# Performance work log

Measured on AMD Instinct MI355X. Metric: run time of the kernel, lower is better.

## Reference

```python
import jax, jax.numpy as jnp
import numpy as np

B, C, IMG, P = 32, 3, 224, 16
D, H, L, F, NCLS = 768, 12, 12, 3072, 1000
NP = (IMG // P) ** 2  # 196
DH = D // H  # 64
EPS = 1e-5


def _ln(x, g, b):
    m = jnp.mean(x, axis=-1, keepdims=True)
    v = jnp.mean(jnp.square(x - m), axis=-1, keepdims=True)
    return (x - m) * jax.lax.rsqrt(v + EPS) * g + b


def setup_inputs() -> dict:
    key = jax.random.key(0)
    ks = iter(jax.random.split(key, 32))
    s = 0.02
    rn = lambda shape: jax.random.normal(next(ks), shape, dtype=jnp.float32) * s
    inp = {
        "x": jax.random.normal(next(ks), (B, C, IMG, IMG), dtype=jnp.float32),
        "Wp": rn((P * P * C, D)), "bp": jnp.zeros((D,), jnp.float32),
        "cls": rn((1, 1, D)), "pos": rn((1, NP + 1, D)),
        # per-layer stacked params (leading dim L)
        "ln1_g": jnp.ones((L, D), jnp.float32), "ln1_b": jnp.zeros((L, D), jnp.float32),
        "Wq": rn((L, H, D, DH)), "bq": jnp.zeros((L, H, DH), jnp.float32),
        "Wk": rn((L, H, D, DH)), "bk": jnp.zeros((L, H, DH), jnp.float32),
        "Wv": rn((L, H, D, DH)), "bv": jnp.zeros((L, H, DH), jnp.float32),
        "Wo": rn((L, D, D)), "bo": jnp.zeros((L, D), jnp.float32),
        "ln2_g": jnp.ones((L, D), jnp.float32), "ln2_b": jnp.zeros((L, D), jnp.float32),
        "W1": rn((L, D, F)), "b1": jnp.zeros((L, F), jnp.float32),
        "W2": rn((L, F, D)), "b2": jnp.zeros((L, D), jnp.float32),
        # classification head
        "hln_g": jnp.ones((D,), jnp.float32), "hln_b": jnp.zeros((D,), jnp.float32),
        "hW1": rn((D, D)), "hb1": jnp.zeros((D,), jnp.float32),
        "hW2": rn((D, NCLS)), "hb2": jnp.zeros((NCLS,), jnp.float32),
    }
    return inp


def _vit(x, Wp, bp, cls, pos, ln1_g, ln1_b, Wq, bq, Wk, bk, Wv, bv, Wo, bo,
         ln2_g, ln2_b, W1, b1, W2, b2, hln_g, hln_b, hW1, hb1, hW2, hb2):
    b = x.shape[0]
    g = IMG // P
    # nn.Unfold(k=16, s=16): channel order (c, kh, kw), patch order (ph, pw)
    patches = x.reshape(b, C, g, P, g, P).transpose(0, 2, 4, 1, 3, 5).reshape(b, NP, C * P * P)
    h = patches @ Wp + bp  # [b, NP, D]
    h = jnp.concatenate([jnp.broadcast_to(cls, (b, 1, D)), h], axis=1) + pos  # [b, S, D]

    scale = 1.0 / jnp.sqrt(jnp.asarray(DH, h.dtype))

    def step(h, p):
        g1, b1_, wq, bq_, wk, bk_, wv, bv_, wo, bo_, g2, b2_, w1, bb1, w2, bb2 = p
        xn = _ln(h, g1, b1_)
        q = jnp.einsum('bsd,hde->bhse', xn, wq) + bq_[:, None, :]
        k = jnp.einsum('bsd,hde->bhse', xn, wk) + bk_[:, None, :]
        v = jnp.einsum('bsd,hde->bhse', xn, wv) + bv_[:, None, :]
        scores = jnp.einsum('bhse,bhte->bhst', q, k) * scale
        attn = jax.nn.softmax(scores, axis=-1)
        o = jnp.einsum('bhst,bhte->bhse', attn, v)  # [b,H,S,DH]
        o = o.transpose(0, 2, 1, 3).reshape(b, -1, D)  # concat heads
        h = o @ wo + bo_ + h
        xn = _ln(h, g2, b2_)
        h = jax.nn.gelu(xn @ w1 + bb1, approximate=False) @ w2 + bb2 + h
        return h, None

    params = (ln1_g, ln1_b, Wq, bq, Wk, bk, Wv, bv, Wo, bo, ln2_g, ln2_b, W1, b1, W2, b2)
    h, _ = jax.lax.scan(step, h, params)

    c = h[:, 0, :]
    c = _ln(c, hln_g, hln_b)
    return jax.nn.gelu(c @ hW1 + hb1, approximate=False) @ hW2 + hb2


def reference(x, Wp, bp, cls, pos, ln1_g, ln1_b, Wq, bq, Wk, bk, Wv, bv, Wo, bo,
              ln2_g, ln2_b, W1, b1, W2, b2, hln_g, hln_b, hW1, hb1, hW2, hb2):
    return _vit(x, Wp, bp, cls, pos, ln1_g, ln1_b, Wq, bq, Wk, bk, Wv, bv, Wo, bo,
                ln2_g, ln2_b, W1, b1, W2, b2, hln_g, hln_b, hW1, hb1, hW2, hb2)
```

## Files before the change

### kernel.cpp

```cpp
#include <hip/hip_runtime.h>

typedef unsigned short u16;
typedef __attribute__((ext_vector_type(8))) short short8;
typedef __attribute__((ext_vector_type(4))) float f32x4;

#define NTOK 6304
#define SP 197

#define OFF_WQKVT 0L
#define OFF_WOT   42467328L
#define OFF_W1T   56623104L
#define OFF_W2T   113246208L
#define OFF_WPT   169869312L
#define OFF_BQKV  171048960L
#define OFF_H     171159552L
#define OFF_XN    190525440L
#define OFF_QKV   200208384L
#define OFF_SC    229257216L
#define OFF_PM1   288867840L
#define OFF_VT    327599616L
#define OFF_CN    340182528L
#define OFF_T1    340280832L
#define WS_NEEDED 340379136L

__device__ __forceinline__ u16 f2bf(float x) {
  unsigned int u = __float_as_uint(x);
  u += 0x7fffu + ((u >> 16) & 1u);
  return (u16)(u >> 16);
}

__device__ __forceinline__ float gelu_f(float x) {
  return 0.5f * x * (1.0f + erff(x * 0.70710678118654752f));
}

__device__ __forceinline__ void gload_lds16(const void* g, void* l) {
  __builtin_amdgcn_global_load_lds(
      (const __attribute__((address_space(1))) unsigned int*)g,
      (__attribute__((address_space(3))) unsigned int*)l, 16, 0, 0);
}

template <int BM, int BN, int WM, int WN, bool BIAS, bool GELU, bool RES,
          bool OBF16, bool REMAP>
__global__ __launch_bounds__(WM * WN * 64, 2) void gemm2(
    const u16* __restrict__ A, int lda,
    const u16* __restrict__ Bm, int ldb,
    void* Cv, int ldc,
    const float* __restrict__ bias, const float* res, int ldres,
    int M, int N, int K, int tilesN) {
  constexpr int THREADS = WM * WN * 64;
  constexpr int TM = BM / WM, TN = BN / WN;
  constexpr int FM = TM / 16, FN = TN / 16;
  constexpr int APT = (BM * 8) / THREADS;
  constexpr int BPT = (BN * 8) / THREADS;
  constexpr int ABYTES = BM * 128;
  constexpr int BUF = ABYTES + BN * 128;
  __shared__ __align__(16) char smem[2 * BUF];

  const int t = threadIdx.x;
  const int l = t & 63;
  const int lr = l & 15, kb = (l >> 4) & 3;
  const int wid = t >> 6;
  const int wr = wid / WN, wc = wid % WN;

  const int nwg = gridDim.x;
  const int orig = blockIdx.x;
  const int q8 = nwg >> 3, r8 = nwg & 7;
  const int xcd = orig & 7, loc = orig >> 3;
  const int wg =
      (xcd < r8 ? xcd * (q8 + 1) : r8 * (q8 + 1) + (xcd - r8) * q8) + loc;
  const int tn = wg % tilesN, tm = wg / tilesN;
  const int m0 = tm * BM, n0 = tn * BN;
  const int Mm1 = M - 1, Nm1 = N - 1;

  const f32x4 zf = {0.f, 0.f, 0.f, 0.f};
  f32x4 acc[FM][FN];
#pragma unroll
  for (int fm = 0; fm < FM; ++fm)
#pragma unroll
    for (int fn = 0; fn < FN; ++fn) acc[fm][fn] = zf;

  auto stage = [&](int kt, int d) {
    const int k0 = kt << 6;
    char* base = smem + d * BUF;
#pragma unroll
    for (int p = 0; p < APT; ++p) {
      int idx = p * THREADS + t;
      int r = idx >> 3, cl = idx & 7;
      int rr = m0 + r;
      rr = rr > Mm1 ? Mm1 : rr;
      gload_lds16(A + (long)rr * lda + k0 + ((cl ^ (r & 7)) << 3),
                  base + ((p * THREADS + (t & ~63)) << 4));
    }
    char* bbase = base + ABYTES;
#pragma unroll
    for (int p = 0; p < BPT; ++p) {
      int idx = p * THREADS + t;
      int r = idx >> 3, cl = idx & 7;
      int rr = n0 + r;
      rr = rr > Nm1 ? Nm1 : rr;
      gload_lds16(Bm + (long)rr * ldb + k0 + ((cl ^ (r & 7)) << 3),
                  bbase + ((p * THREADS + (t & ~63)) << 4));
    }
  };

  const int nt = K >> 6;
  stage(0, 0);
  __syncthreads();

  for (int kt = 0; kt < nt; ++kt) {
    if (kt + 1 < nt) stage(kt + 1, (kt + 1) & 1);
    const char* Ab = smem + (kt & 1) * BUF;
    const char* Bb = Ab + ABYTES;
#pragma unroll
    for (int kk = 0; kk < 2; ++kk) {
      const int ch = ((((kk << 2) | kb) ^ (lr & 7)) << 4);
      short8 af[FM], bf[FN];
#pragma unroll
      for (int fm = 0; fm < FM; ++fm)
        af[fm] = *(const short8*)(Ab + (wr * TM + fm * 16 + lr) * 128 + ch);
#pragma unroll
      for (int fn = 0; fn < FN; ++fn)
        bf[fn] = *(const short8*)(Bb + (wc * TN + fn * 16 + lr) * 128 + ch);
#pragma unroll
      for (int fm = 0; fm < FM; ++fm)
#pragma unroll
        for (int fn = 0; fn < FN; ++fn)
          acc[fm][fn] = __builtin_amdgcn_mfma_f32_16x16x32_bf16(af[fm], bf[fn],
                                                                acc[fm][fn], 0, 0, 0);
    }
    __syncthreads();
  }

#pragma unroll
  for (int fn = 0; fn < FN; ++fn) {
    const int gc = n0 + wc * TN + fn * 16 + lr;
    if (gc >= N) continue;
    const float bv = BIAS ? bias[gc] : 0.0f;
#pragma unroll
    for (int fm = 0; fm < FM; ++fm) {
#pragma unroll
      for (int j = 0; j < 4; ++j) {
        const int gr = m0 + wr * TM + fm * 16 + kb * 4 + j;
        if (gr >= M) continue;
        float v = acc[fm][fn][j] + bv;
        if (RES) v += res[(long)gr * ldres + gc];
        if (GELU) v = gelu_f(v);
        long orow = gr;
        if (REMAP) orow = (long)(gr / 196) * 197 + (gr % 196) + 1;
        if (OBF16)
          ((u16*)Cv)[orow * (long)ldc + gc] = f2bf(v);
        else
          ((float*)Cv)[orow * (long)ldc + gc] = v;
      }
    }
  }
}

__global__ __launch_bounds__(256) void k_attn(const u16* __restrict__ qkv,
                                              u16* __restrict__ o) {
  __shared__ __align__(16) u16 Kb[208 * 72];
  __shared__ __align__(16) u16 Vt[64 * 232];
  __shared__ __align__(16) u16 Pl[4][16 * 232];

  const int t = threadIdx.x;
  const int z = blockIdx.x;
  const int b = z / 12, hh = z % 12;
  const long qbase = (long)b * SP * 2304 + hh * 64;

#pragma unroll
  for (int p = 0; p < 7; ++p) {
    int idx = p * 256 + t;
    int row = idx >> 3, c = idx & 7;
    short8 kv = {0, 0, 0, 0, 0, 0, 0, 0};
    short8 vv = {0, 0, 0, 0, 0, 0, 0, 0};
    if (row < SP) {
      kv = *(const short8*)(qkv + qbase + 768 + (long)row * 2304 + c * 8);
      vv = *(const short8*)(qkv + qbase + 1536 + (long)row * 2304 + c * 8);
    }
    if (row < 208) *(short8*)(&Kb[row * 72 + c * 8]) = kv;
#pragma unroll
    for (int j = 0; j < 8; ++j) Vt[(c * 8 + j) * 232 + row] = ((const u16*)&vv)[j];
  }
  __syncthreads();

  const int l = t & 63, wid = t >> 6;
  const int lr = l & 15, kb = l >> 4;
  u16* Pw = Pl[wid];
  const f32x4 zf = {0.f, 0.f, 0.f, 0.f};

  for (int st = wid; st < 13; st += 4) {
    int qrow = st * 16 + lr;
    qrow = qrow > SP - 1 ? SP - 1 : qrow;
    short8 qf[2];
#pragma unroll
    for (int kk = 0; kk < 2; ++kk)
      qf[kk] = *(const short8*)(qkv + qbase + (long)qrow * 2304 + kk * 32 + kb * 8);

    f32x4 s[13];
#pragma unroll
    for (int nt = 0; nt < 13; ++nt) {
      s[nt] = zf;
#pragma unroll
      for (int kk = 0; kk < 2; ++kk) {
        short8 kf = *(const short8*)(&Kb[(nt * 16 + lr) * 72 + kk * 32 + kb * 8]);
        s[nt] = __builtin_amdgcn_mfma_f32_16x16x32_bf16(qf[kk], kf, s[nt], 0, 0, 0);
      }
    }

    float mx[4] = {-1e30f, -1e30f, -1e30f, -1e30f};
#pragma unroll
    for (int nt = 0; nt < 13; ++nt) {
      const bool pred = (nt < 12) | (lr < 5);
#pragma unroll
      for (int j = 0; j < 4; ++j) {
        float v = s[nt][j] * 0.125f;
        s[nt][j] = v;
        if (pred) mx[j] = fmaxf(mx[j], v);
      }
    }
#pragma unroll
    for (int o4 = 1; o4 < 16; o4 <<= 1)
#pragma unroll
      for (int j = 0; j < 4; ++j) mx[j] = fmaxf(mx[j], __shfl_xor(mx[j], o4));
    float sum[4] = {0.f, 0.f, 0.f, 0.f};
#pragma unroll
    for (int nt = 0; nt < 13; ++nt) {
      const bool pred = (nt < 12) | (lr < 5);
#pragma unroll
      for (int j = 0; j < 4; ++j) {
        float p = pred ? __expf(s[nt][j] - mx[j]) : 0.f;
        s[nt][j] = p;
        sum[j] += p;
      }
    }
#pragma unroll
    for (int o4 = 1; o4 < 16; o4 <<= 1)
#pragma unroll
      for (int j = 0; j < 4; ++j) sum[j] += __shfl_xor(sum[j], o4);
    float inv[4];
#pragma unroll
    for (int j = 0; j < 4; ++j) inv[j] = 1.0f / sum[j];

#pragma unroll
    for (int nt = 0; nt < 13; ++nt)
#pragma unroll
      for (int j = 0; j < 4; ++j)
        Pw[(kb * 4 + j) * 232 + nt * 16 + lr] = f2bf(s[nt][j] * inv[j]);
#pragma unroll
    for (int j = 0; j < 4; ++j) Pw[(kb * 4 + j) * 232 + 208 + lr] = 0;

    short8 pf[7];
#pragma unroll
    for (int kk = 0; kk < 7; ++kk)
      pf[kk] = *(const short8*)(&Pw[lr * 232 + kk * 32 + kb * 8]);
#pragma unroll
    for (int dt = 0; dt < 4; ++dt) {
      f32x4 oacc = zf;
#pragma unroll
      for (int kk = 0; kk < 7; ++kk) {
        short8 vf = *(const short8*)(&Vt[(dt * 16 + lr) * 232 + kk * 32 + kb * 8]);
        oacc = __builtin_amdgcn_mfma_f32_16x16x32_bf16(pf[kk], vf, oacc, 0, 0, 0);
      }
#pragma unroll
      for (int j = 0; j < 4; ++j) {
        int qr = st * 16 + kb * 4 + j;
        if (qr < SP)
          o[((long)b * SP + qr) * 768 + hh * 64 + dt * 16 + lr] = f2bf(oacc[j]);
      }
    }
  }
}

__global__ void k_wt64(const float* __restrict__ W, u16* __restrict__ out,
                       int sel) {
  __shared__ float tile[32][33];
  const int z = blockIdx.z;
  const int ly = z / 12, hh = z % 12;
  const float* ip = W + (long)z * 768 * 64;
  u16* op = out + (long)ly * 2304 * 768 + ((long)sel * 768 + hh * 64) * 768;
  const int c0 = blockIdx.x * 32, r0 = blockIdx.y * 32;
  const int tx = threadIdx.x, ty = threadIdx.y;
#pragma unroll
  for (int i = 0; i < 4; ++i)
    tile[ty + i * 8][tx] = ip[(long)(r0 + ty + i * 8) * 64 + c0 + tx];
  __syncthreads();
#pragma unroll
  for (int i = 0; i < 4; ++i)
    op[(long)(c0 + ty + i * 8) * 768 + r0 + tx] = f2bf(tile[tx][ty + i * 8]);
}

__global__ void k_bqkv(const float* __restrict__ bq, const float* __restrict__ bk,
                       const float* __restrict__ bv, float* __restrict__ out) {
  int idx = blockIdx.x * 256 + threadIdx.x;
  if (idx >= 27648) return;
  int c = idx % 2304, ly = idx / 2304;
  int sel = c / 768, cc = c % 768;
  const float* b = sel == 0 ? bq : (sel == 1 ? bk : bv);
  out[idx] = b[ly * 768 + cc];
}

__global__ void k_transpose(const float* __restrict__ in, u16* __restrict__ out,
                            int R, int C) {
  __shared__ float tile[32][33];
  long zoff = (long)blockIdx.z * R * C;
  const float* ip = in + zoff;
  u16* op = out + zoff;
  int c0 = blockIdx.x * 32, r0 = blockIdx.y * 32;
  int tx = threadIdx.x, ty = threadIdx.y;
#pragma unroll
  for (int i = 0; i < 4; ++i)
    tile[ty + i * 8][tx] = ip[(long)(r0 + ty + i * 8) * C + c0 + tx];
  __syncthreads();
#pragma unroll
  for (int i = 0; i < 4; ++i)
    op[(long)(c0 + ty + i * 8) * R + r0 + tx] = f2bf(tile[tx][ty + i * 8]);
}

__global__ void k_patchify(const float* __restrict__ x, u16* __restrict__ out) {
  long idx = (long)blockIdx.x * 256 + threadIdx.x;
  int f = (int)(idx % 768);
  long rp = idx / 768;
  int p = (int)(rp % 196), b = (int)(rp / 196);
  int gy = p / 14, gx = p % 14;
  int c = f >> 8, rem = f & 255;
  int i = rem >> 4, j = rem & 15;
  out[idx] = f2bf(x[(((long)b * 3 + c) * 224 + gy * 16 + i) * 224 + gx * 16 + j]);
}

__global__ void k_add_pos(float* h, const float* __restrict__ cls,
                          const float* __restrict__ pos) {
  long idx = (long)blockIdx.x * 256 + threadIdx.x;
  int d = (int)(idx % 768);
  long rs = idx / 768;
  int s = (int)(rs % 197);
  if (s == 0)
    h[idx] = cls[d] + pos[d];
  else
    h[idx] += pos[(long)s * 768 + d];
}

__global__ __launch_bounds__(256) void k_ln(const float* __restrict__ in,
                                            const float* __restrict__ g,
                                            const float* __restrict__ b,
                                            u16* __restrict__ out, int rows) {
  int w = threadIdx.x >> 6, l = threadIdx.x & 63;
  int row = blockIdx.x * 4 + w;
  if (row >= rows) return;
  const float4* ip = (const float4*)(in + (long)row * 768);
  float4 v[3];
  float s = 0.f, sq = 0.f;
#pragma unroll
  for (int i = 0; i < 3; ++i) {
    v[i] = ip[i * 64 + l];
    s += v[i].x + v[i].y + v[i].z + v[i].w;
    sq += v[i].x * v[i].x + v[i].y * v[i].y + v[i].z * v[i].z + v[i].w * v[i].w;
  }
#pragma unroll
  for (int o = 1; o < 64; o <<= 1) {
    s += __shfl_xor(s, o);
    sq += __shfl_xor(sq, o);
  }
  const float m = s * (1.f / 768.f);
  const float rs = rsqrtf(sq * (1.f / 768.f) - m * m + 1e-5f);
  ushort4* op = (ushort4*)(out + (long)row * 768);
#pragma unroll
  for (int i = 0; i < 3; ++i) {
    int c4 = (i * 64 + l) * 4;
    float4 gv = *(const float4*)(g + c4);
    float4 bv = *(const float4*)(b + c4);
    ushort4 o4;
    o4.x = f2bf((v[i].x - m) * rs * gv.x + bv.x);
    o4.y = f2bf((v[i].y - m) * rs * gv.y + bv.y);
    o4.z = f2bf((v[i].z - m) * rs * gv.z + bv.z);
    o4.w = f2bf((v[i].w - m) * rs * gv.w + bv.w);
    op[i * 64 + l] = o4;
  }
}

__global__ void k_head_ln(const float* __restrict__ h, const float* __restrict__ g,
                          const float* __restrict__ b, float* __restrict__ out) {
  const int bb = blockIdx.x, l = threadIdx.x;
  const float4* ip = (const float4*)(h + (long)bb * 197 * 768);
  float4 v[3];
  float s = 0.f, sq = 0.f;
#pragma unroll
  for (int i = 0; i < 3; ++i) {
    v[i] = ip[i * 64 + l];
    s += v[i].x + v[i].y + v[i].z + v[i].w;
    sq += v[i].x * v[i].x + v[i].y * v[i].y + v[i].z * v[i].z + v[i].w * v[i].w;
  }
#pragma unroll
  for (int o = 1; o < 64; o <<= 1) {
    s += __shfl_xor(s, o);
    sq += __shfl_xor(sq, o);
  }
  const float m = s * (1.f / 768.f);
  const float rs = rsqrtf(sq * (1.f / 768.f) - m * m + 1e-5f);
  float4* op = (float4*)(out + bb * 768);
#pragma unroll
  for (int i = 0; i < 3; ++i) {
    int c4 = (i * 64 + l) * 4;
    float4 gv = *(const float4*)(g + c4);
    float4 bv = *(const float4*)(b + c4);
    float4 o4;
    o4.x = (v[i].x - m) * rs * gv.x + bv.x;
    o4.y = (v[i].y - m) * rs * gv.y + bv.y;
    o4.z = (v[i].z - m) * rs * gv.z + bv.z;
    o4.w = (v[i].w - m) * rs * gv.w + bv.w;
    op[i * 64 + l] = o4;
  }
}

template <bool GELU>
__global__ __launch_bounds__(256) void k_head_gemm(
    const float* __restrict__ in, const float* __restrict__ W,
    const float* __restrict__ bias, float* __restrict__ out, int K, int N) {
  __shared__ float partial[4][64];
  const int b = blockIdx.y;
  const int cl = threadIdx.x & 63;
  const int c = blockIdx.x * 64 + cl;
  const int kp = threadIdx.x >> 6;
  const int kc = K >> 2;
  float s = 0.f;
  if (c < N) {
    const float* ip = in + (long)b * K + kp * kc;
    const float* wp = W + (long)(kp * kc) * N + c;
    for (int k = 0; k < kc; ++k) s = fmaf(ip[k], wp[(long)k * N], s);
  }
  partial[kp][cl] = s;
  __syncthreads();
  if (kp == 0 && c < N) {
    float v = partial[0][cl] + partial[1][cl] + partial[2][cl] + partial[3][cl] +
              bias[c];
    if (GELU) v = gelu_f(v);
    out[(long)b * N + c] = v;
  }
}

extern "C" void kernel_launch(void* const* d_in, const int* in_sizes, int n_in,
                              void* d_out, int out_size, void* d_ws, size_t ws_size,
                              hipStream_t stream) {
  (void)in_sizes; (void)n_in; (void)out_size;
  if ((long)ws_size < WS_NEEDED) return;

  const float* x = (const float*)d_in[0];
  const float* Wp = (const float*)d_in[1];
  const float* bp = (const float*)d_in[2];
  const float* cls = (const float*)d_in[3];
  const float* pos = (const float*)d_in[4];
  const float* ln1g = (const float*)d_in[5];
  const float* ln1b = (const float*)d_in[6];
  const float* Wq = (const float*)d_in[7];
  const float* bq = (const float*)d_in[8];
  const float* Wk = (const float*)d_in[9];
  const float* bk = (const float*)d_in[10];
  const float* Wv = (const float*)d_in[11];
  const float* bv = (const float*)d_in[12];
  const float* Wo = (const float*)d_in[13];
  const float* bo = (const float*)d_in[14];
  const float* ln2g = (const float*)d_in[15];
  const float* ln2b = (const float*)d_in[16];
  const float* W1 = (const float*)d_in[17];
  const float* b1 = (const float*)d_in[18];
  const float* W2 = (const float*)d_in[19];
  const float* b2 = (const float*)d_in[20];
  const float* hlng = (const float*)d_in[21];
  const float* hlnb = (const float*)d_in[22];
  const float* hW1 = (const float*)d_in[23];
  const float* hb1 = (const float*)d_in[24];
  const float* hW2 = (const float*)d_in[25];
  const float* hb2 = (const float*)d_in[26];

  char* ws = (char*)d_ws;
  u16* wqkvt = (u16*)(ws + OFF_WQKVT);
  u16* wot = (u16*)(ws + OFF_WOT);
  u16* w1t = (u16*)(ws + OFF_W1T);
  u16* w2t = (u16*)(ws + OFF_W2T);
  u16* wpt = (u16*)(ws + OFF_WPT);
  float* bqkv = (float*)(ws + OFF_BQKV);
  float* h = (float*)(ws + OFF_H);
  u16* xn = (u16*)(ws + OFF_XN);
  u16* qkv = (u16*)(ws + OFF_QKV);
  u16* pbuf = qkv;
  u16* m1 = (u16*)(ws + OFF_PM1);
  float* cn = (float*)(ws + OFF_CN);
  float* t1 = (float*)(ws + OFF_T1);

  k_wt64<<<dim3(2, 24, 144), dim3(32, 8), 0, stream>>>(Wq, wqkvt, 0);
  k_wt64<<<dim3(2, 24, 144), dim3(32, 8), 0, stream>>>(Wk, wqkvt, 1);
  k_wt64<<<dim3(2, 24, 144), dim3(32, 8), 0, stream>>>(Wv, wqkvt, 2);
  k_bqkv<<<108, 256, 0, stream>>>(bq, bk, bv, bqkv);
  k_transpose<<<dim3(24, 24, 12), dim3(32, 8), 0, stream>>>(Wo, wot, 768, 768);
  k_transpose<<<dim3(96, 24, 12), dim3(32, 8), 0, stream>>>(W1, w1t, 768, 3072);
  k_transpose<<<dim3(24, 96, 12), dim3(32, 8), 0, stream>>>(W2, w2t, 3072, 768);
  k_transpose<<<dim3(24, 24, 1), dim3(32, 8), 0, stream>>>(Wp, wpt, 768, 768);

  k_patchify<<<18816, 256, 0, stream>>>(x, pbuf);
  gemm2<128, 128, 2, 2, true, false, false, false, true><<<294, 256, 0, stream>>>(
      pbuf, 768, wpt, 768, h, 768, bp, nullptr, 0, 6272, 768, 768, 6);
  k_add_pos<<<18912, 256, 0, stream>>>(h, cls, pos);

  for (int ly = 0; ly < 12; ++ly) {
    k_ln<<<1576, 256, 0, stream>>>(h, ln1g + ly * 768, ln1b + ly * 768, xn, NTOK);
    gemm2<128, 128, 2, 2, true, false, false, true, false><<<900, 256, 0, stream>>>(
        xn, 768, wqkvt + (long)ly * 2304 * 768, 768, qkv, 2304,
        bqkv + ly * 2304, nullptr, 0, NTOK, 2304, 768, 18);
    k_attn<<<384, 256, 0, stream>>>(qkv, xn);
    gemm2<128, 128, 2, 2, true, false, true, false, false><<<300, 256, 0, stream>>>(
        xn, 768, wot + (long)ly * 768 * 768, 768, h, 768,
        bo + ly * 768, h, 768, NTOK, 768, 768, 6);
    k_ln<<<1576, 256, 0, stream>>>(h, ln2g + ly * 768, ln2b + ly * 768, xn, NTOK);
    gemm2<128, 128, 2, 2, true, true, false, true, false><<<1200, 256, 0, stream>>>(
        xn, 768, w1t + (long)ly * 3072 * 768, 768, m1, 3072,
        b1 + ly * 3072, nullptr, 0, NTOK, 3072, 768, 24);
    gemm2<128, 128, 2, 2, true, false, true, false, false><<<300, 256, 0, stream>>>(
        m1, 3072, w2t + (long)ly * 768 * 3072, 3072, h, 768,
        b2 + ly * 768, h, 768, NTOK, 768, 3072, 6);
  }

  k_head_ln<<<32, 64, 0, stream>>>(h, hlng, hlnb, cn);
  k_head_gemm<true><<<dim3(12, 32), 256, 0, stream>>>(cn, hW1, hb1, t1, 768, 768);
  k_head_gemm<false><<<dim3(16, 32), 256, 0, stream>>>(t1, hW2, hb2, (float*)d_out,
                                                       768, 1000);
}
```

Before: 3.497 ms.

## Add single-buffered 3-wave-occupancy GEMM for QKV and FC1, vectorize pos add

```diff
diff --git a/kernel.cpp b/kernel.cpp
--- a/kernel.cpp
+++ b/kernel.cpp
@@ -37,6 +37,103 @@
   __builtin_amdgcn_global_load_lds(
       (const __attribute__((address_space(1))) unsigned int*)g,
       (__attribute__((address_space(3))) unsigned int*)l, 16, 0, 0);
+}
+
+template <bool BIAS, bool GELU, bool RES, bool OBF16, bool REMAP>
+__global__ __launch_bounds__(256, 3) void gemm_k(
+    const u16* __restrict__ A, int lda,
+    const u16* __restrict__ Bm, int ldb,
+    void* Cv, int ldc,
+    const float* __restrict__ bias, const float* res, int ldres,
+    int M, int N, int K, int tilesN) {
+  __shared__ float4 smemv[2048];
+  char* smem = (char*)smemv;
+
+  const int t = threadIdx.x;
+  const int nwg = gridDim.x;
+  const int orig = blockIdx.x;
+  const int q8 = nwg >> 3, r8 = nwg & 7;
+  const int xcd = orig & 7, loc = orig >> 3;
+  const int wg =
+      (xcd < r8 ? xcd * (q8 + 1) : r8 * (q8 + 1) + (xcd - r8) * q8) + loc;
+  const int tn = wg % tilesN, tm = wg / tilesN;
+  const int m0 = tm * 128, n0 = tn * 128;
+  const int l = t & 63;
+  const int lr = l & 15, kb = l >> 4;
+  const int wr = (t >> 7) & 1, wc = (t >> 6) & 1;
+
+  const f32x4 zf = {0.f, 0.f, 0.f, 0.f};
+  f32x4 acc[4][4];
+#pragma unroll
+  for (int m = 0; m < 4; ++m)
+#pragma unroll
+    for (int n = 0; n < 4; ++n) acc[m][n] = zf;
+
+  auto stage = [&](const u16* src, int ld, int row0, int maxrow, int k0,
+                   char* ldsbase) {
+#pragma unroll
+    for (int p = 0; p < 4; ++p) {
+      int idx = p * 256 + t;
+      int r = idx >> 3;
+      int cl = idx & 7;
+      int cg = cl ^ (r & 7);
+      int rr = row0 + r;
+      rr = rr > maxrow ? maxrow : rr;
+      gload_lds16(src + (long)rr * ld + k0 + cg * 8,
+                  ldsbase + (long)(p * 256 + (t & ~63)) * 16);
+    }
+  };
+
+  const int KT = K >> 6;
+  for (int kt = 0; kt < KT; ++kt) {
+    stage(A, lda, m0, M - 1, kt * 64, smem);
+    stage(Bm, ldb, n0, N - 1, kt * 64, smem + 16384);
+    __syncthreads();
+    const char* Ab = smem;
+    const char* Bb = smem + 16384;
+#pragma unroll
+    for (int kk = 0; kk < 2; ++kk) {
+      const int cla = ((kk << 2) + kb) ^ (lr & 7);
+      short8 af[4], bfv[4];
+#pragma unroll
+      for (int m = 0; m < 4; ++m)
+        af[m] = *(const short8*)(Ab + ((wr * 64 + m * 16 + lr) * 128 + cla * 16));
+#pragma unroll
+      for (int n = 0; n < 4; ++n)
+        bfv[n] = *(const short8*)(Bb + ((wc * 64 + n * 16 + lr) * 128 + cla * 16));
+#pragma unroll
+      for (int m = 0; m < 4; ++m)
+#pragma unroll
+        for (int n = 0; n < 4; ++n)
+          acc[m][n] = __builtin_amdgcn_mfma_f32_16x16x32_bf16(af[m], bfv[n],
+                                                              acc[m][n], 0, 0, 0);
+    }
+    __syncthreads();
+  }
+
+#pragma unroll
+  for (int n = 0; n < 4; ++n) {
+    const int gc = n0 + wc * 64 + n * 16 + lr;
+    if (gc >= N) continue;
+    const float bv = BIAS ? bias[gc] : 0.0f;
+#pragma unroll
+    for (int m = 0; m < 4; ++m) {
+#pragma unroll
+      for (int j = 0; j < 4; ++j) {
+        const int gr = m0 + wr * 64 + m * 16 + kb * 4 + j;
+        if (gr >= M) continue;
+        float v = acc[m][n][j] + bv;
+        if (RES) v += res[(long)gr * ldres + gc];
+        if (GELU) v = gelu_f(v);
+        long orow = gr;
+        if (REMAP) orow = (long)(gr / 196) * 197 + (gr % 196) + 1;
+        if (OBF16)
+          ((u16*)Cv)[orow * (long)ldc + gc] = f2bf(v);
+        else
+          ((float*)Cv)[orow * (long)ldc + gc] = v;
+      }
+    }
+  }
 }
 
 template <int BM, int BN, int WM, int WN, bool BIAS, bool GELU, bool RES,
@@ -330,13 +427,21 @@
 __global__ void k_add_pos(float* h, const float* __restrict__ cls,
                           const float* __restrict__ pos) {
   long idx = (long)blockIdx.x * 256 + threadIdx.x;
-  int d = (int)(idx % 768);
-  long rs = idx / 768;
+  int d4 = (int)(idx % 192);
+  long rs = idx / 192;
   int s = (int)(rs % 197);
-  if (s == 0)
-    h[idx] = cls[d] + pos[d];
-  else
-    h[idx] += pos[(long)s * 768 + d];
+  float4* hp = (float4*)h;
+  const float4* pp = (const float4*)pos;
+  if (s == 0) {
+    const float4* cp = (const float4*)cls;
+    float4 v = cp[d4], w = pp[d4];
+    v.x += w.x; v.y += w.y; v.z += w.z; v.w += w.w;
+    hp[idx] = v;
+  } else {
+    float4 v = hp[idx], w = pp[(long)s * 192 + d4];
+    v.x += w.x; v.y += w.y; v.z += w.z; v.w += w.w;
+    hp[idx] = v;
+  }
 }
 
 __global__ __launch_bounds__(256) void k_ln(const float* __restrict__ in,
@@ -498,11 +603,11 @@
   k_patchify<<<18816, 256, 0, stream>>>(x, pbuf);
   gemm2<128, 128, 2, 2, true, false, false, false, true><<<294, 256, 0, stream>>>(
       pbuf, 768, wpt, 768, h, 768, bp, nullptr, 0, 6272, 768, 768, 6);
-  k_add_pos<<<18912, 256, 0, stream>>>(h, cls, pos);
+  k_add_pos<<<4728, 256, 0, stream>>>(h, cls, pos);
 
   for (int ly = 0; ly < 12; ++ly) {
     k_ln<<<1576, 256, 0, stream>>>(h, ln1g + ly * 768, ln1b + ly * 768, xn, NTOK);
-    gemm2<128, 128, 2, 2, true, false, false, true, false><<<900, 256, 0, stream>>>(
+    gemm_k<true, false, false, true, false><<<900, 256, 0, stream>>>(
         xn, 768, wqkvt + (long)ly * 2304 * 768, 768, qkv, 2304,
         bqkv + ly * 2304, nullptr, 0, NTOK, 2304, 768, 18);
     k_attn<<<384, 256, 0, stream>>>(qkv, xn);
@@ -510,7 +615,7 @@
         xn, 768, wot + (long)ly * 768 * 768, 768, h, 768,
         bo + ly * 768, h, 768, NTOK, 768, 768, 6);
     k_ln<<<1576, 256, 0, stream>>>(h, ln2g + ly * 768, ln2b + ly * 768, xn, NTOK);
-    gemm2<128, 128, 2, 2, true, true, false, true, false><<<1200, 256, 0, stream>>>(
+    gemm_k<true, true, false, true, false><<<1200, 256, 0, stream>>>(
         xn, 768, w1t + (long)ly * 3072 * 768, 768, m1, 3072,
         b1 + ly * 3072, nullptr, 0, NTOK, 3072, 768, 24);
     gemm2<128, 128, 2, 2, true, false, true, false, false><<<300, 256, 0, stream>>>(
```

Result: faster. 3.260 ms (-6.8%).
